# Performance work log

Measured on AMD Instinct MI355X. Metric: run time of the kernel, lower is better.

Reference implementation:

```python
import jax, jax.numpy as jnp
from jax import lax
import numpy as np

B, P, KPASS = 1024, 128, 1


def _mlp(x, Wa, ba, Wb, bb):
    # torch nn.Sequential(Linear, ReLU, Linear); weights stored as [in, out]
    return jnp.maximum(x @ Wa + ba, 0.0) @ Wb + bb


def setup_inputs() -> dict:
    key = jax.random.key(0)
    ks = jax.random.split(key, 9)
    fdim = P + (P - 1) ** 2  # col/diag learner input dim
    h = P - 1
    A = jax.random.normal(ks[0], (B, P, P), jnp.float32)
    # well-conditioned SPD input (module inverts it immediately)
    Theta = A @ jnp.swapaxes(A, -1, -2) / P + 2.0 * jnp.eye(P, dtype=jnp.float32)
    s = 0.02
    return {
        'Theta': Theta,
        'W1': s * jax.random.normal(ks[1], (fdim, h), jnp.float32),
        'b1': s * jax.random.normal(ks[2], (h,), jnp.float32),
        'W2': s * jax.random.normal(ks[3], (h, h), jnp.float32),
        'b2': s * jax.random.normal(ks[4], (h,), jnp.float32),
        'D1': s * jax.random.normal(ks[5], (fdim, h), jnp.float32),
        'd1': s * jax.random.normal(ks[6], (h,), jnp.float32),
        'D2': s * jax.random.normal(ks[7], (h, 1), jnp.float32),
        'd2': s * jax.random.normal(ks[8], (1,), jnp.float32),
    }


def _one_pass(Theta, W, W1, b1, W2, b2, D1, d1, D2, d2):
    b, p = Theta.shape[0], Theta.shape[-1]
    base = jnp.arange(p - 1)
    cols = jnp.arange(p)

    def gather(M, col, idxm):
        # M_11 [b,p-1,p-1], m_12 [b,p-1], m_22 [b]
        return (M[:, idxm[:, None], idxm[None, :]], M[:, idxm, col], M[:, col, col])

    # ---- first column sweep: learned off-diagonal update (no cross-col dep on Theta) ----
    def step1(carry, col):
        Delta, _ = carry
        idxm = base + (base >= col).astype(base.dtype)  # indices minus col
        T11, t12, t22 = gather(Theta, col, idxm)
        feats = jnp.concatenate([T11.reshape(b, -1), t12, t22[:, None]], -1)
        t12n = _mlp(feats, W1, b1, W2, b2)
        d = t12n - t12
        Delta = Delta.at[:, idxm, col].set(d).at[:, col, idxm].set(d)
        return (Delta, t12n), None

    init = (jnp.zeros_like(Theta), jnp.zeros((b, p - 1), Theta.dtype))
    (Delta, t12n_stale), _ = lax.scan(step1, init, cols)
    # NOTE: t12n_stale = theta_12_next from the LAST column — faithful to the original,
    # which reuses the leftover Python variable inside the second loop.
    Theta = Theta + Delta

    # ---- second column sweep: diagonal/Schur bookkeeping + rank-1 W updates (sequential) ----
    def step2(carry, col):
        Th, Wc = carry
        idxm = base + (base >= col).astype(base.dtype)
        T11, t12, t22 = gather(Th, col, idxm)
        W11, w12, w22 = gather(Wc, col, idxm)
        feats = jnp.concatenate([T11.reshape(b, -1), t12, t22[:, None]], -1)
        inv11 = W11 - (1.0 / w22)[:, None, None] * w12[:, :, None] * w12[:, None, :]
        schur = jnp.einsum('bi,bij,bj->b', t12, inv11, t12)
        gy = jnp.exp(_mlp(feats, D1, d1, D2, d2))[:, 0]
        t22n = gy + schur  # feeds only the (detached) W update, as in the original
        Th = Th + Delta    # faithful: original re-adds Delta every column
        quad = jnp.einsum('bi,bij,bj->b', t12n_stale, inv11, t12n_stale)
        w22n = 1.0 / (t22n - quad)
        w12n = jnp.einsum('b,bij,bj->bi', -w22n, inv11, t12n_stale)
        Wn11 = inv11 + (1.0 / w22n)[:, None, None] * w12n[:, :, None] * w12n[:, None, :]
        Wc = Wc.at[:, idxm[:, None], idxm[None, :]].set(Wn11)
        Wc = Wc.at[:, idxm, col].set(w12n).at[:, col, idxm].set(w12n).at[:, col, col].set(w22n)
        Wc = lax.stop_gradient(Wc)  # original .detach()-es all W writes
        return (Th, Wc), None

    (Theta, W), _ = lax.scan(step2, (Theta, W), cols)
    return Theta, W


def reference(Theta, W1, b1, W2, b2, D1, d1, D2, d2):
    W = lax.stop_gradient(jnp.linalg.inv(Theta))
    for _ in range(KPASS):
        Theta, W = _one_pass(Theta, W, W1, b1, W2, b2, D1, d1, D2, d2)
    return Theta
```

## Files before the change

kernel.cpp:

```cpp
#include <hip/hip_runtime.h>

#define PP 128
#define H  127
#define NV 384
#define NB 1024


__global__ __launch_bounds__(128) void build_wp(const float* __restrict__ W1,
                                                float* __restrict__ WP) {
  int bid = blockIdx.x;
  int k = bid >> 7, c = bid & 127;
  int o = threadIdx.x;
  float v1 = 0.f, v2 = 0.f, v3 = 0.f, v4 = 0.f;
  if (o < H) {
    if (k <= 126) {
      if (c < k)       v1 = W1[(k*H + c)*H + o]     + W1[(c*H + k)*H + o];
      else if (c == k) v1 = W1[(k*H + k)*H + o];
      else             v1 = W1[(k*H + (c-1))*H + o] + W1[((c-1)*H + k)*H + o];
    }
    if (k >= 1 && c < k)
      v2 = W1[(c*H + (k-1))*H + o] + W1[((k-1)*H + c)*H + o];
    if (k >= 1) {
      if (c > k)       v3 = W1[((k-1)*H + (c-1))*H + o] + W1[((c-1)*H + (k-1))*H + o];
      else if (c == k) v3 = W1[((k-1)*H + (k-1))*H + o];
    }
    if (c < k)       v4 = W1[(16129 + c)*H + o];
    else if (c == k) v4 = W1[16256*H + o];
    else             v4 = W1[(16129 + (c-1))*H + o];
  }
  size_t base = (size_t)(k*PP + c) * NV;
  WP[base + o]       = v1 - v2;
  WP[base + 128 + o] = v3;
  WP[base + 256 + o] = v4 - v2;
}

__global__ __launch_bounds__(256) void transpose_th(const float* __restrict__ Th,
                                                    float* __restrict__ Tht,
                                                    int bbase, int BC) {
  __shared__ float tile[64][65];
  int c0 = blockIdx.x * 64, b0 = blockIdx.y * 64, k = blockIdx.z;
  int tid = threadIdx.x;
  int c4 = (tid & 15) * 4, r = tid >> 4;
  for (int rr = 0; rr < 64; rr += 16) {
    float4 v = *(const float4*)&Th[((size_t)(bbase + b0 + r + rr) * PP + k) * PP + c0 + c4];
    tile[r + rr][c4 + 0] = v.x; tile[r + rr][c4 + 1] = v.y;
    tile[r + rr][c4 + 2] = v.z; tile[r + rr][c4 + 3] = v.w;
  }
  __syncthreads();
  int b4 = (tid & 15) * 4, cq = tid >> 4;
  for (int cc = 0; cc < 64; cc += 16) {
    int c = cq + cc;
    float4 v = make_float4(tile[b4 + 0][c], tile[b4 + 1][c],
                           tile[b4 + 2][c], tile[b4 + 3][c]);
    *(float4*)&Tht[((size_t)k * PP + c0 + c) * BC + b0 + b4] = v;
  }
}

__global__ __launch_bounds__(256, 4) void pgemm(const float* __restrict__ Tht,
                                                const float* __restrict__ WP,
                                                float* __restrict__ P, int BC) {
  __shared__ float As[32 * 128];
  __shared__ float Bs[32 * 128];
  int nt = blockIdx.x, bt = blockIdx.y, k = blockIdx.z;
  int n0 = nt * 128;
  int tid = threadIdx.x;
  int tx = tid & 15, ty = tid >> 4;
  float acc[8][8] = {};
  for (int kc = 0; kc < 128; kc += 32) {
    {
      int p4 = (tid & 31) * 4, cc = tid >> 5;
      #pragma unroll
      for (int c2 = 0; c2 < 32; c2 += 8) {
        *(float4*)&As[(cc + c2) * 128 + p4] =
            *(const float4*)&Tht[((size_t)k * PP + kc + cc + c2) * BC + bt * 128 + p4];
        *(float4*)&Bs[(cc + c2) * 128 + p4] =
            *(const float4*)&WP[(size_t)(k * PP + kc + cc + c2) * NV + n0 + p4];
      }
    }
    __syncthreads();
    #pragma unroll
    for (int kk = 0; kk < 32; ++kk) {
      float4 a0 = *(const float4*)&As[kk * 128 + ty * 4];
      float4 a1 = *(const float4*)&As[kk * 128 + 64 + ty * 4];
      float4 b0 = *(const float4*)&Bs[kk * 128 + tx * 4];
      float4 b1 = *(const float4*)&Bs[kk * 128 + 64 + tx * 4];
      float av[8] = {a0.x, a0.y, a0.z, a0.w, a1.x, a1.y, a1.z, a1.w};
      float bv[8] = {b0.x, b0.y, b0.z, b0.w, b1.x, b1.y, b1.z, b1.w};
      #pragma unroll
      for (int i = 0; i < 8; ++i)
        #pragma unroll
        for (int j = 0; j < 8; ++j) acc[i][j] = fmaf(av[i], bv[j], acc[i][j]);
    }
    __syncthreads();
  }
  #pragma unroll
  for (int i = 0; i < 8; ++i) {
    int row = (i < 4) ? ty * 4 + i : 64 + ty * 4 + (i - 4);
    size_t base = ((size_t)(bt * 128 + row) * PP + k) * NV + n0;
    *(float4*)&P[base + tx * 4]      = make_float4(acc[i][0], acc[i][1], acc[i][2], acc[i][3]);
    *(float4*)&P[base + 64 + tx * 4] = make_float4(acc[i][4], acc[i][5], acc[i][6], acc[i][7]);
  }
}

__global__ __launch_bounds__(512, 4) void scan_c(const float* __restrict__ P,
                                                 float* __restrict__ At,
                                                 const float* __restrict__ b1) {
  __shared__ float zl[128 * 127];
  float* ftot = zl;
  float* btot = zl + 512;
  int bl = blockIdx.x;
  int o = threadIdx.x & 127, s = threadIdx.x >> 7;
  const float* Pb = P + (size_t)bl * PP * NV;
  float q[32], r[32];
  float fa = 0.f, ba = 0.f;
  #pragma unroll
  for (int t = 0; t < 32; ++t) {
    int col = s * 32 + t;
    q[t] = Pb[col * NV + o];
    r[t] = Pb[col * NV + 128 + o];
    fa += q[t]; ba += r[t];
  }
  ftot[s * 128 + o] = fa;
  btot[s * 128 + o] = ba;
  __syncthreads();
  float fc = 0.f, bc = 0.f;
  for (int t = 0; t < s; ++t)     fc += ftot[t * 128 + o];
  for (int t = s + 1; t < 4; ++t) bc += btot[t * 128 + o];
  float b1v = (o < H) ? b1[o] : 0.f;
  __syncthreads();
  float qp = 0.f, rinc = 0.f;
  #pragma unroll
  for (int t = 0; t < 32; ++t) {
    int col = s * 32 + t;
    float L = Pb[col * NV + 256 + o];
    rinc += r[t];
    float z = b1v + fc + qp + bc + (ba - rinc) + L;
    qp += q[t];
    if (o < H) zl[col * 127 + o] = fmaxf(z, 0.f);
  }
  __syncthreads();
  float* Ab = At + (size_t)bl * PP * PP;
  for (int idx = threadIdx.x; idx < PP * PP; idx += 512) {
    int oo = idx >> 7, col = idx & 127;
    Ab[idx] = (oo < H) ? zl[col * 127 + oo] : 0.f;
  }
}

__global__ __launch_bounds__(256, 4) void gemm2(const float* __restrict__ At,
                                                const float* __restrict__ W2,
                                                const float* __restrict__ b2,
                                                const float* __restrict__ Th,
                                                float* __restrict__ out, int bbase) {
  __shared__ float smem[PP * H];
  float* Al  = smem;
  float* W2l = smem + 4096;
  int bl = blockIdx.x, b = bbase + bl;
  int tid = threadIdx.x;
  int tn = tid & 15, tm = tid >> 4;
  const float* Ab = At + (size_t)bl * PP * PP;
  float acc[8][8];
  #pragma unroll
  for (int i = 0; i < 8; ++i)
    #pragma unroll
    for (int j = 0; j < 8; ++j) {
      int oc = (j < 4) ? tn * 4 + j : 64 + tn * 4 + (j - 4);
      acc[i][j] = (oc < H) ? b2[oc] : 0.f;
    }
  for (int kc = 0; kc < 128; kc += 32) {
    {
      int c4 = (tid & 31) * 4, jj = tid >> 5;
      #pragma unroll
      for (int j2 = 0; j2 < 32; j2 += 8)
        *(float4*)&Al[(jj + j2) * 128 + c4] =
            *(const float4*)&Ab[(size_t)(kc + jj + j2) * 128 + c4];
      int oo = tid & 127, j0 = tid >> 7;
      #pragma unroll
      for (int j2 = 0; j2 < 32; j2 += 2) {
        int row = kc + j0 + j2;
        W2l[(j0 + j2) * 128 + oo] = (row < H && oo < H) ? W2[(size_t)row * H + oo] : 0.f;
      }
    }
    __syncthreads();
    #pragma unroll
    for (int kk = 0; kk < 32; ++kk) {
      float4 a0 = *(const float4*)&Al[kk * 128 + tm * 4];
      float4 a1 = *(const float4*)&Al[kk * 128 + 64 + tm * 4];
      float4 b0 = *(const float4*)&W2l[kk * 128 + tn * 4];
      float4 b1 = *(const float4*)&W2l[kk * 128 + 64 + tn * 4];
      float av[8] = {a0.x, a0.y, a0.z, a0.w, a1.x, a1.y, a1.z, a1.w};
      float bv[8] = {b0.x, b0.y, b0.z, b0.w, b1.x, b1.y, b1.z, b1.w};
      #pragma unroll
      for (int i = 0; i < 8; ++i)
        #pragma unroll
        for (int j = 0; j < 8; ++j) acc[i][j] = fmaf(av[i], bv[j], acc[i][j]);
    }
    __syncthreads();
  }
  #pragma unroll
  for (int i = 0; i < 8; ++i) {
    int row = (i < 4) ? tm * 4 + i : 64 + tm * 4 + (i - 4);
    #pragma unroll
    for (int j = 0; j < 8; ++j) {
      int oc = (j < 4) ? tn * 4 + j : 64 + tn * 4 + (j - 4);
      if (oc < H) smem[row * H + oc] = acc[i][j];
    }
  }
  __syncthreads();
  const float* Tb = Th + (size_t)b * PP * PP;
  float* ob = out + (size_t)b * PP * PP;
  for (int it = 0; it < 64; ++it) {
    int idx = tid + 256 * it;
    int rr = idx >> 7, cc = idx & 127;
    float th = Tb[idx];
    float val;
    if (rr == cc) val = th;
    else {
      int M = rr > cc ? rr : cc, m = rr > cc ? cc : rr;
      val = 129.f * smem[M * H + m] - 128.f * th;
    }
    ob[idx] = val;
  }
}

extern "C" void kernel_launch(void* const* d_in, const int* in_sizes, int n_in,
                              void* d_out, int out_size, void* d_ws, size_t ws_size,
                              hipStream_t stream) {
  const float* Th = (const float*)d_in[0];
  const float* W1 = (const float*)d_in[1];
  const float* b1 = (const float*)d_in[2];
  const float* W2 = (const float*)d_in[3];
  const float* b2 = (const float*)d_in[4];
  float* out = (float*)d_out;

  const size_t wp_elems = (size_t)PP * PP * NV;
  int BC = 1024;
  while (BC > 128 &&
         (wp_elems + (size_t)BC * PP * PP + (size_t)BC * PP * NV) * 4 > ws_size)
    BC >>= 1;

  float* WP  = (float*)d_ws;
  float* Tht = WP + wp_elems;
  float* Pb  = Tht + (size_t)BC * PP * PP;

  build_wp<<<dim3(16384), dim3(128), 0, stream>>>(W1, WP);
  for (int bb = 0; bb < NB; bb += BC) {
    transpose_th<<<dim3(2, BC / 64, 128), dim3(256), 0, stream>>>(Th, Tht, bb, BC);
    pgemm<<<dim3(3, BC / 128, 128), dim3(256), 0, stream>>>(Tht, WP, Pb, BC);
    scan_c<<<dim3(BC), dim3(512), 0, stream>>>(Pb, Tht, b1);
    gemm2<<<dim3(BC), dim3(256), 0, stream>>>(Tht, W2, b2, Th, out, bb);
  }
}
```

Baseline: 549.5 us.

## Split gemm2 into GEMM-to-buffer plus tiled symmetric scatter kernel

The fused gemm2 kernel, which staged the full 128x127 result in shared memory (about 64 KB) before scattering, becomes two kernels. The GEMM now writes its tile directly to global memory through float4 stores and uses only 32 KB of shared memory, which may allow more resident blocks. A separate scatter kernel processes the three lower/diagonal 64x64 tile pairs with a padded shared transpose and vectorized reads and writes of Theta. The cost is a round trip of the intermediate through global memory and one extra kernel launch.

```diff
diff --git a/kernel.cpp b/kernel.cpp
--- a/kernel.cpp
+++ b/kernel.cpp
@@ -146,15 +146,13 @@
   }
 }
 
-__global__ __launch_bounds__(256, 4) void gemm2(const float* __restrict__ At,
-                                                const float* __restrict__ W2,
-                                                const float* __restrict__ b2,
-                                                const float* __restrict__ Th,
-                                                float* __restrict__ out, int bbase) {
-  __shared__ float smem[PP * H];
-  float* Al  = smem;
-  float* W2l = smem + 4096;
-  int bl = blockIdx.x, b = bbase + bl;
+__global__ __launch_bounds__(256, 4) void gemm_t12(const float* __restrict__ At,
+                                                   const float* __restrict__ W2,
+                                                   const float* __restrict__ b2,
+                                                   float* __restrict__ t12) {
+  __shared__ float Al[32 * 128];
+  __shared__ float W2l[32 * 128];
+  int bl = blockIdx.x;
   int tid = threadIdx.x;
   int tn = tid & 15, tm = tid >> 4;
   const float* Ab = At + (size_t)bl * PP * PP;
@@ -199,26 +197,66 @@
   #pragma unroll
   for (int i = 0; i < 8; ++i) {
     int row = (i < 4) ? tm * 4 + i : 64 + tm * 4 + (i - 4);
-    #pragma unroll
-    for (int j = 0; j < 8; ++j) {
-      int oc = (j < 4) ? tn * 4 + j : 64 + tn * 4 + (j - 4);
-      if (oc < H) smem[row * H + oc] = acc[i][j];
-    }
-  }
-  __syncthreads();
+    size_t base = ((size_t)bl * PP + row) * PP;
+    *(float4*)&t12[base + tn * 4]      = make_float4(acc[i][0], acc[i][1], acc[i][2], acc[i][3]);
+    *(float4*)&t12[base + 64 + tn * 4] = make_float4(acc[i][4], acc[i][5], acc[i][6], acc[i][7]);
+  }
+}
+
+__global__ __launch_bounds__(256) void scatter(const float* __restrict__ t12,
+                                               const float* __restrict__ Th,
+                                               float* __restrict__ out, int bbase) {
+  __shared__ float St[64 * 65];
+  int pi = blockIdx.x, bl = blockIdx.y, b = bbase + bl;
+  int ti = (pi == 2) ? 1 : 0, tj = (pi == 0) ? 0 : 1;
+  int R0 = tj * 64, C0 = ti * 64;
+  const float* tb = t12 + (size_t)bl * PP * PP;
   const float* Tb = Th + (size_t)b * PP * PP;
   float* ob = out + (size_t)b * PP * PP;
-  for (int it = 0; it < 64; ++it) {
-    int idx = tid + 256 * it;
-    int rr = idx >> 7, cc = idx & 127;
-    float th = Tb[idx];
-    float val;
-    if (rr == cc) val = th;
-    else {
-      int M = rr > cc ? rr : cc, m = rr > cc ? cc : rr;
-      val = 129.f * smem[M * H + m] - 128.f * th;
-    }
-    ob[idx] = val;
+  int t = threadIdx.x;
+  int cc4 = (t & 15) * 4, rr = t >> 4;
+  float4 s[4];
+  #pragma unroll
+  for (int g = 0; g < 4; ++g) {
+    int r = rr + g * 16;
+    s[g] = *(const float4*)&tb[(R0 + r) * PP + C0 + cc4];
+    St[(cc4 + 0) * 65 + r] = s[g].x;
+    St[(cc4 + 1) * 65 + r] = s[g].y;
+    St[(cc4 + 2) * 65 + r] = s[g].z;
+    St[(cc4 + 3) * 65 + r] = s[g].w;
+  }
+  if (pi == 1) {
+    #pragma unroll
+    for (int g = 0; g < 4; ++g) {
+      int r = R0 + rr + g * 16;
+      float4 th = *(const float4*)&Tb[r * PP + C0 + cc4];
+      float4 v = make_float4(129.f * s[g].x - 128.f * th.x,
+                             129.f * s[g].y - 128.f * th.y,
+                             129.f * s[g].z - 128.f * th.z,
+                             129.f * s[g].w - 128.f * th.w);
+      *(float4*)&ob[r * PP + C0 + cc4] = v;
+    }
+  }
+  __syncthreads();
+  #pragma unroll
+  for (int g = 0; g < 4; ++g) {
+    int rr2 = rr + g * 16;
+    int r = C0 + rr2;
+    int cb = R0 + cc4;
+    float4 th = *(const float4*)&Tb[r * PP + cb];
+    float thv[4] = {th.x, th.y, th.z, th.w};
+    float v[4];
+    #pragma unroll
+    for (int i = 0; i < 4; ++i) {
+      int cc2 = cc4 + i;
+      float x;
+      if (pi == 1)            x = 129.f * St[rr2 * 65 + cc2] - 128.f * thv[i];
+      else if (cc2 > rr2)     x = 129.f * St[rr2 * 65 + cc2] - 128.f * thv[i];
+      else if (cc2 < rr2)     x = 129.f * St[cc2 * 65 + rr2] - 128.f * thv[i];
+      else                    x = thv[i];
+      v[i] = x;
+    }
+    *(float4*)&ob[r * PP + cb] = make_float4(v[0], v[1], v[2], v[3]);
   }
 }
 
@@ -247,6 +285,7 @@
     transpose_th<<<dim3(2, BC / 64, 128), dim3(256), 0, stream>>>(Th, Tht, bb, BC);
     pgemm<<<dim3(3, BC / 128, 128), dim3(256), 0, stream>>>(Tht, WP, Pb, BC);
     scan_c<<<dim3(BC), dim3(512), 0, stream>>>(Pb, Tht, b1);
-    gemm2<<<dim3(BC), dim3(256), 0, stream>>>(Tht, W2, b2, Th, out, bb);
-  }
-}
+    gemm_t12<<<dim3(BC), dim3(256), 0, stream>>>(Tht, W2, b2, Pb);
+    scatter<<<dim3(3, BC), dim3(256), 0, stream>>>(Pb, Th, out, bb);
+  }
+}
```

Measured after the change: 677.5 us. 1.23x slower.
